# Performance work log

Measured on AMD Instinct MI355X. Metric: run time of the kernel, lower is better.

Reference implementation:

```python
import jax, jax.numpy as jnp
import numpy as np

B, S, H = 4, 2048, 1024
NH = 1                     # source code only type-checks with 1 head (see notes)
DH = H // NH               # head dim == hidden size
DT = 32                    # distance_type
LN_EPS = 1e-12


def setup_inputs() -> dict:
    key = jax.random.key(0)
    ks = jax.random.split(key, 12)
    sd = 0.02
    hidden_states = jax.random.normal(ks[0], (B, S, H), dtype=jnp.float32)
    attention_mask = jnp.zeros((B, 1, 1, S), dtype=jnp.float32)
    word_word_relation = jax.random.randint(ks[1], (B, S, S), 0, DT, dtype=jnp.int64)
    dist_emb = sd * jax.random.normal(ks[2], (DT, H), dtype=jnp.float32)
    dist_emb = dist_emb.at[0].set(0.0)  # padding_idx=0
    return {
        "hidden_states": hidden_states,
        "attention_mask": attention_mask,
        "word_word_relation": word_word_relation,
        "Wq": sd * jax.random.normal(ks[3], (H, H), dtype=jnp.float32),
        "bq": jnp.zeros((H,), dtype=jnp.float32),
        "Wk": sd * jax.random.normal(ks[4], (H, H), dtype=jnp.float32),
        "bk": jnp.zeros((H,), dtype=jnp.float32),
        "Wv": sd * jax.random.normal(ks[5], (H, H), dtype=jnp.float32),
        "bv": jnp.zeros((H,), dtype=jnp.float32),
        "dist_emb": dist_emb,
        "Wo": sd * jax.random.normal(ks[6], (H, H), dtype=jnp.float32),
        "bo": jnp.zeros((H,), dtype=jnp.float32),
        "ln_g": jnp.ones((H,), dtype=jnp.float32),
        "ln_b": jnp.zeros((H,), dtype=jnp.float32),
    }


def _split_heads(x):
    # [B,S,H] -> [B,NH,S,DH]
    return x.reshape(B, S, NH, DH).transpose(0, 2, 1, 3)


def reference(hidden_states, attention_mask, word_word_relation, Wq, bq, Wk, bk,
              Wv, bv, dist_emb, Wo, bo, ln_g, ln_b):
    q = _split_heads(hidden_states @ Wq.T + bq)   # [B,NH,S,DH]
    k = _split_heads(hidden_states @ Wk.T + bk)
    v = _split_heads(hidden_states @ Wv.T + bv)

    # raw QK^T scores [B,NH,S,S]
    scores = jnp.einsum('bhqd,bhkd->bhqk', q, k)

    # query . distance_embedding^T : [B,NH,S,DT]
    word_dot_distance = jnp.einsum('bhqd,td->bhqt', q, dist_emb)

    rel = word_word_relation[:, None, :, :]       # [B,1,S,S]
    # gather per-pair distance score along the distance-type axis
    dist_att = jnp.take_along_axis(word_dot_distance, rel, axis=3)  # [B,NH,S,S]
    mask_out = (rel == 1).astype(scores.dtype)    # keep only relation==1 pairs
    dist_att = dist_att * mask_out

    scores = (scores + dist_att) / jnp.sqrt(jnp.asarray(DH, scores.dtype))
    scores = scores + attention_mask              # additive BERT mask
    probs = jax.nn.softmax(scores, axis=-1)       # dropout p=0 -> identity

    ctx = jnp.einsum('bhqk,bhkd->bhqd', probs, v) # [B,NH,S,DH]
    ctx = ctx.transpose(0, 2, 1, 3).reshape(B, S, H)

    # BertSelfOutput: dense -> residual -> LayerNorm
    attn_out = ctx @ Wo.T + bo
    x = attn_out + hidden_states
    mu = jnp.mean(x, axis=-1, keepdims=True)
    var = jnp.mean(jnp.square(x - mu), axis=-1, keepdims=True)
    out = (x - mu) * jax.lax.rsqrt(var + LN_EPS) * ln_g + ln_b
    return out
```

## Files before the change

### kernel.cpp

```cpp
#include <hip/hip_runtime.h>

#define BM 128
#define BN 128
#define BKH 32

typedef __bf16 bf16x8 __attribute__((ext_vector_type(8)));
typedef __bf16 bf16x4 __attribute__((ext_vector_type(4)));
typedef float f32x4 __attribute__((ext_vector_type(4)));
typedef __bf16 bf16_t;

__device__ __forceinline__ void gl_lds16(const void* g, void* l) {
    __builtin_amdgcn_global_load_lds(
        (const __attribute__((address_space(1))) void*)g,
        (__attribute__((address_space(3))) void*)l, 16, 0, 0);
}

__global__ __launch_bounds__(256)
void cvt_all_kernel(const float* __restrict__ hid,
                    const float* __restrict__ w0, const float* __restrict__ w1,
                    const float* __restrict__ w2, const float* __restrict__ w3,
                    bf16_t* __restrict__ hidb, bf16_t* __restrict__ wb)
{
    const int bid = blockIdx.x;
    const float* src;
    bf16_t* dst;
    size_t off;
    if (bid < 8192) {
        src = hid; dst = hidb; off = (size_t)bid * 1024;
    } else {
        const int i = (bid - 8192) >> 10;
        src = (i == 0) ? w0 : (i == 1) ? w1 : (i == 2) ? w2 : w3;
        dst = wb + (size_t)i * 1024 * 1024;
        off = (size_t)((bid - 8192) & 1023) * 1024;
    }
    const size_t idx = off + threadIdx.x * 4;
    const float4 v = *(const float4*)(src + idx);
    bf16x4 o;
    o[0] = (__bf16)v.x; o[1] = (__bf16)v.y;
    o[2] = (__bf16)v.z; o[3] = (__bf16)v.w;
    *(bf16x4*)(dst + idx) = o;
}

template <int MODE, int SWIZ>
__global__ __launch_bounds__(256)
void gemm_bt(const bf16_t* __restrict__ A, const bf16_t* __restrict__ Bw,
             const float* __restrict__ bias, const float* __restrict__ bias2,
             const float* __restrict__ bias3,
             bf16_t* __restrict__ C, bf16_t* __restrict__ C2,
             int M, int N, int K,
             long long sAz, long long sBz, long long sCz,
             const float* __restrict__ resid,
             int Sdim, int DHdim)
{
    const int bz = blockIdx.z;
    const float* bi = bias;
    if (MODE == 0) {
        Bw += (long long)bz * N * K;
        bi = (bz == 0) ? bias : (bz == 1 ? bias2 : bias3);
        if (bz < 2) C += (long long)bz * sCz;
    } else {
        A += (long long)bz * sAz;
        Bw += (long long)bz * sBz;
        C += (long long)bz * sCz;
    }

    int m0, n0;
    if (SWIZ) {
        const int num_n = N / BN;
        const int pid = blockIdx.x;
        const int group = 8 * num_n;
        const int g = pid / group;
        m0 = (g * 8 + (pid % 8)) * BM;
        n0 = ((pid % group) / 8) * BN;
    } else {
        m0 = blockIdx.y * BM;
        n0 = blockIdx.x * BN;
    }
    const int tid = threadIdx.x;
    const int w = tid >> 6;
    const int lane = tid & 63;
    const int wr = w >> 1;
    const int wc = w & 1;
    const int srow = lane >> 2;
    const int scol = (lane & 3) * 8;
    const int frow = lane & 15;
    const int fk = (lane >> 4) * 8;

    __shared__ bf16_t smem[4 * BM * BKH];
    bf16_t* A0 = smem;
    bf16_t* A1 = smem + BM * BKH;
    bf16_t* B0 = smem + 2 * BM * BKH;
    bf16_t* B1 = smem + 3 * BM * BKH;

    f32x4 acc[4][4];
#pragma unroll
    for (int i = 0; i < 4; ++i)
#pragma unroll
        for (int j = 0; j < 4; ++j) acc[i][j] = (f32x4)0.0f;

    for (int k0 = 0; k0 < K; k0 += 2 * BKH) {
#pragma unroll
        for (int i = 0; i < 2; ++i) {
            const int r = i * 64 + w * 16;
            const bf16_t* ga = A + (size_t)(m0 + r + srow) * K + (k0 + scol);
            const bf16_t* gb = Bw + (size_t)(n0 + r + srow) * K + (k0 + scol);
            gl_lds16(ga,        &A0[r * BKH]);
            gl_lds16(ga + BKH,  &A1[r * BKH]);
            gl_lds16(gb,        &B0[r * BKH]);
            gl_lds16(gb + BKH,  &B1[r * BKH]);
        }
        __syncthreads();
#pragma unroll
        for (int h = 0; h < 2; ++h) {
            const bf16_t* Ah = h ? A1 : A0;
            const bf16_t* Bh = h ? B1 : B0;
            bf16x8 af[4], bfv[4];
#pragma unroll
            for (int t = 0; t < 4; ++t) {
                af[t]  = *(const bf16x8*)&Ah[(wr * 64 + t * 16 + frow) * BKH + fk];
                bfv[t] = *(const bf16x8*)&Bh[(wc * 64 + t * 16 + frow) * BKH + fk];
            }
#pragma unroll
            for (int mt = 0; mt < 4; ++mt)
#pragma unroll
                for (int nt = 0; nt < 4; ++nt)
                    acc[mt][nt] = __builtin_amdgcn_mfma_f32_16x16x32_bf16(
                        af[mt], bfv[nt], acc[mt][nt], 0, 0, 0);
        }
        __syncthreads();
    }

    const int crow = (lane >> 4) * 4;
    const int ccol = lane & 15;

    if (MODE == 0 && bz == 2) {
#pragma unroll
        for (int mt = 0; mt < 4; ++mt) {
            const int mb = m0 + wr * 64 + mt * 16 + crow;
#pragma unroll
            for (int nt = 0; nt < 4; ++nt) {
                const int n = n0 + wc * 64 + nt * 16 + ccol;
                const float bv = bi[n];
                const int b = mb >> 11;
                const int s = mb & 2047;
                union { ushort4 u; bf16_t h[4]; } pk;
#pragma unroll
                for (int r = 0; r < 4; ++r) pk.h[r] = (__bf16)(acc[mt][nt][r] + bv);
                *(ushort4*)&C2[(size_t)b * DHdim * Sdim + (size_t)n * Sdim + s] = pk.u;
            }
        }
        return;
    }

    bf16_t* tw = smem + w * (16 * 72);
    const int r0 = lane >> 3;
    const int cseg = (lane & 7) * 8;

    float bv[4];
    if (MODE == 0 || MODE == 4) {
#pragma unroll
        for (int nt = 0; nt < 4; ++nt)
            bv[nt] = bi[n0 + wc * 64 + nt * 16 + ccol];
    }

#pragma unroll
    for (int mt = 0; mt < 4; ++mt) {
#pragma unroll
        for (int nt = 0; nt < 4; ++nt) {
            const float badd = (MODE == 0 || MODE == 4) ? bv[nt] : 0.0f;
#pragma unroll
            for (int r = 0; r < 4; ++r)
                tw[(crow + r) * 72 + nt * 16 + ccol] = (__bf16)(acc[mt][nt][r] + badd);
        }
        bf16x8 va = *(const bf16x8*)&tw[r0 * 72 + cseg];
        bf16x8 vb = *(const bf16x8*)&tw[(r0 + 8) * 72 + cseg];

        const int gm_a = m0 + wr * 64 + mt * 16 + r0;
        const int gm_b = gm_a + 8;
        const int gn = n0 + wc * 64 + cseg;

        if (MODE == 0 || MODE == 3) {
            *(bf16x8*)&C[(size_t)gm_a * N + gn] = va;
            *(bf16x8*)&C[(size_t)gm_b * N + gn] = vb;
        } else {
            const float4 xa0 = *(const float4*)&resid[(size_t)gm_a * N + gn];
            const float4 xa1 = *(const float4*)&resid[(size_t)gm_a * N + gn + 4];
            const float4 xb0 = *(const float4*)&resid[(size_t)gm_b * N + gn];
            const float4 xb1 = *(const float4*)&resid[(size_t)gm_b * N + gn + 4];
            bf16x8 oa, ob;
            oa[0] = (__bf16)((float)va[0] + xa0.x);
            oa[1] = (__bf16)((float)va[1] + xa0.y);
            oa[2] = (__bf16)((float)va[2] + xa0.z);
            oa[3] = (__bf16)((float)va[3] + xa0.w);
            oa[4] = (__bf16)((float)va[4] + xa1.x);
            oa[5] = (__bf16)((float)va[5] + xa1.y);
            oa[6] = (__bf16)((float)va[6] + xa1.z);
            oa[7] = (__bf16)((float)va[7] + xa1.w);
            ob[0] = (__bf16)((float)vb[0] + xb0.x);
            ob[1] = (__bf16)((float)vb[1] + xb0.y);
            ob[2] = (__bf16)((float)vb[2] + xb0.z);
            ob[3] = (__bf16)((float)vb[3] + xb0.w);
            ob[4] = (__bf16)((float)vb[4] + xb1.x);
            ob[5] = (__bf16)((float)vb[5] + xb1.y);
            ob[6] = (__bf16)((float)vb[6] + xb1.z);
            ob[7] = (__bf16)((float)vb[7] + xb1.w);
            *(bf16x8*)&C[(size_t)gm_a * N + gn] = oa;
            *(bf16x8*)&C[(size_t)gm_b * N + gn] = ob;
        }
    }
}

__global__ __launch_bounds__(256)
void softmax_kernel(bf16_t* __restrict__ sc, const int* __restrict__ rel,
                    const bf16_t* __restrict__ q, const float* __restrict__ de,
                    const float* __restrict__ mask)
{
    constexpr int S = 2048, H = 1024;
    const int row = blockIdx.x;
    const int b = row >> 11;
    const int tid = threadIdx.x;
    const int w = tid >> 6, lane = tid & 63;
    __shared__ float rd1[4], rmax[4], rsum[4];

    const bf16x4 q4 = *(const bf16x4*)(q + (size_t)row * H + tid * 4);
    const float4 e4 = *(const float4*)(de + H + tid * 4);
    float pd = (float)q4[0] * e4.x + (float)q4[1] * e4.y
             + (float)q4[2] * e4.z + (float)q4[3] * e4.w;
#pragma unroll
    for (int off = 32; off; off >>= 1) pd += __shfl_xor(pd, off, 64);
    if (lane == 0) rd1[w] = pd;
    __syncthreads();
    const float d1s = (rd1[0] + rd1[1] + rd1[2] + rd1[3]) * 0.03125f;

    bf16_t* p = sc + (size_t)row * S;
    const bf16x8 x = *(const bf16x8*)(p + tid * 8);
    const int4 rl0 = *(const int4*)&rel[(size_t)row * S + tid * 8];
    const int4 rl1 = *(const int4*)&rel[(size_t)row * S + tid * 8 + 4];
    const float4 mk0 = *(const float4*)&mask[(size_t)b * S + tid * 8];
    const float4 mk1 = *(const float4*)&mask[(size_t)b * S + tid * 8 + 4];
    const int rls[8] = {rl0.x, rl0.y, rl0.z, rl0.w, rl1.x, rl1.y, rl1.z, rl1.w};
    const float mks[8] = {mk0.x, mk0.y, mk0.z, mk0.w, mk1.x, mk1.y, mk1.z, mk1.w};
    float v[8];
    float mx = -1e30f;
#pragma unroll
    for (int j = 0; j < 8; ++j) {
        v[j] = (float)x[j] * 0.03125f + mks[j] + (rls[j] == 1 ? d1s : 0.0f);
        mx = fmaxf(mx, v[j]);
    }
#pragma unroll
    for (int off = 32; off; off >>= 1) mx = fmaxf(mx, __shfl_xor(mx, off, 64));
    if (lane == 0) rmax[w] = mx;
    __syncthreads();
    mx = fmaxf(fmaxf(rmax[0], rmax[1]), fmaxf(rmax[2], rmax[3]));
    float sum = 0.0f;
#pragma unroll
    for (int j = 0; j < 8; ++j) { v[j] = __expf(v[j] - mx); sum += v[j]; }
#pragma unroll
    for (int off = 32; off; off >>= 1) sum += __shfl_xor(sum, off, 64);
    if (lane == 0) rsum[w] = sum;
    __syncthreads();
    sum = rsum[0] + rsum[1] + rsum[2] + rsum[3];
    const float inv = 1.0f / sum;
    bf16x8 o;
#pragma unroll
    for (int j = 0; j < 8; ++j) o[j] = (__bf16)(v[j] * inv);
    *(bf16x8*)(p + tid * 8) = o;
}

__global__ __launch_bounds__(256)
void ln_kernel(const bf16_t* __restrict__ x, const float* __restrict__ gamma,
               const float* __restrict__ beta, float* __restrict__ out)
{
    const int H = 1024;
    const size_t row = blockIdx.x;
    const int tid = threadIdx.x;
    const int w = tid >> 6, lane = tid & 63;
    bf16x4 xv = *(const bf16x4*)(x + row * H + tid * 4);
    float v[4] = {(float)xv[0], (float)xv[1], (float)xv[2], (float)xv[3]};
    float s = 0.0f, s2 = 0.0f;
#pragma unroll
    for (int j = 0; j < 4; ++j) { s += v[j]; s2 += v[j] * v[j]; }
#pragma unroll
    for (int off = 32; off; off >>= 1) {
        s += __shfl_xor(s, off, 64);
        s2 += __shfl_xor(s2, off, 64);
    }
    __shared__ float rs[4], rs2[4];
    if (lane == 0) { rs[w] = s; rs2[w] = s2; }
    __syncthreads();
    s  = rs[0] + rs[1] + rs[2] + rs[3];
    s2 = rs2[0] + rs2[1] + rs2[2] + rs2[3];
    const float mu  = s * (1.0f / H);
    const float var = s2 * (1.0f / H) - mu * mu;
    const float inv = rsqrtf(var + 1e-12f);
    float4 o;
    const int c = tid * 4;
    o.x = (v[0] - mu) * inv * gamma[c + 0] + beta[c + 0];
    o.y = (v[1] - mu) * inv * gamma[c + 1] + beta[c + 1];
    o.z = (v[2] - mu) * inv * gamma[c + 2] + beta[c + 2];
    o.w = (v[3] - mu) * inv * gamma[c + 3] + beta[c + 3];
    *(float4*)(out + row * H + tid * 4) = o;
}

extern "C" void kernel_launch(void* const* d_in, const int* in_sizes, int n_in,
                              void* d_out, int out_size, void* d_ws, size_t ws_size,
                              hipStream_t stream)
{
    constexpr int B = 4, S = 2048, H = 1024;
    const float* hid = (const float*)d_in[0];
    const float* am  = (const float*)d_in[1];
    const int*   rel = (const int*)d_in[2];
    const float* Wq  = (const float*)d_in[3];
    const float* bq  = (const float*)d_in[4];
    const float* Wk  = (const float*)d_in[5];
    const float* bk  = (const float*)d_in[6];
    const float* Wv  = (const float*)d_in[7];
    const float* bv  = (const float*)d_in[8];
    const float* de  = (const float*)d_in[9];
    const float* Wo  = (const float*)d_in[10];
    const float* bo  = (const float*)d_in[11];
    const float* lng = (const float*)d_in[12];
    const float* lnb = (const float*)d_in[13];
    float* out = (float*)d_out;

    char* ws = (char*)d_ws;
    const int n_tok = B * S;
    const size_t MB = 1024 * 1024;
    bf16_t* hidb = (bf16_t*)(ws);
    bf16_t* Wqb  = (bf16_t*)(ws + 16 * MB);
    bf16_t* Wob  = (bf16_t*)(ws + 22 * MB);
    bf16_t* qb   = (bf16_t*)(ws + 24 * MB);
    bf16_t* kb   = (bf16_t*)(ws + 40 * MB);
    bf16_t* vT   = (bf16_t*)(ws + 56 * MB);
    bf16_t* ctx  = (bf16_t*)(ws + 72 * MB);
    bf16_t* sc   = (bf16_t*)(ws + 88 * MB);
    bf16_t* xb   = (bf16_t*)(ws + 88 * MB);

    const dim3 blk(256);
    cvt_all_kernel<<<dim3(8192 + 4 * 1024), blk, 0, stream>>>(
        hid, Wq, Wk, Wv, Wo, hidb, Wqb);

    gemm_bt<0, 1><<<dim3(64 * 8, 1, 3), blk, 0, stream>>>(
        hidb, Wqb, bq, bk, bv, qb, vT, n_tok, H, H,
        0, 0, (long long)n_tok * H,
        nullptr, S, H);
    gemm_bt<3, 0><<<dim3(S / BN, S / BM, B), blk, 0, stream>>>(
        qb, kb, nullptr, nullptr, nullptr, sc, nullptr, S, S, H,
        (long long)S * H, (long long)S * H, (long long)S * S,
        nullptr, S, H);
    softmax_kernel<<<dim3(B * S), blk, 0, stream>>>(sc, rel, qb, de, am);
    gemm_bt<3, 0><<<dim3(H / BN, S / BM, B), blk, 0, stream>>>(
        sc, vT, nullptr, nullptr, nullptr, ctx, nullptr, S, H, S,
        (long long)S * S, (long long)H * S, (long long)S * H,
        nullptr, S, H);
    gemm_bt<4, 0><<<dim3(H / BN, n_tok / BM, 1), blk, 0, stream>>>(
        ctx, Wob, bo, nullptr, nullptr, xb, nullptr, n_tok, H, H, 0, 0, 0,
        hid, S, H);
    ln_kernel<<<dim3(n_tok), blk, 0, stream>>>(xb, lng, lnb, out);
}
```

Measured before the change: 379.3 us.

## Rework GEMM into 256x128 tiles with triple-buffered swizzled LDS pipeline

```diff
diff --git a/kernel.cpp b/kernel.cpp
--- a/kernel.cpp
+++ b/kernel.cpp
@@ -1,18 +1,25 @@
 #include <hip/hip_runtime.h>
 
-#define BM 128
+#define BM 256
 #define BN 128
-#define BKH 32
+#define BK 64
+#define NBUF 3
+#define BUFELEMS ((BM + BN) * BK)
 
 typedef __bf16 bf16x8 __attribute__((ext_vector_type(8)));
 typedef __bf16 bf16x4 __attribute__((ext_vector_type(4)));
 typedef float f32x4 __attribute__((ext_vector_type(4)));
 typedef __bf16 bf16_t;
 
+#define MFMA16(a, b, c) __builtin_amdgcn_mfma_f32_16x16x32_bf16((a), (b), (c), 0, 0, 0)
+
 __device__ __forceinline__ void gl_lds16(const void* g, void* l) {
     __builtin_amdgcn_global_load_lds(
         (const __attribute__((address_space(1))) void*)g,
         (__attribute__((address_space(3))) void*)l, 16, 0, 0);
+}
+__device__ __forceinline__ void barrier_mem() {
+    asm volatile("s_barrier" ::: "memory");
 }
 
 __global__ __launch_bounds__(256)
@@ -41,8 +48,8 @@
     *(bf16x4*)(dst + idx) = o;
 }
 
-template <int MODE, int SWIZ>
-__global__ __launch_bounds__(256)
+template <int MODE>
+__global__ __launch_bounds__(512, 2)
 void gemm_bt(const bf16_t* __restrict__ A, const bf16_t* __restrict__ Bw,
              const float* __restrict__ bias, const float* __restrict__ bias2,
              const float* __restrict__ bias3,
@@ -63,34 +70,33 @@
         Bw += (long long)bz * sBz;
         C += (long long)bz * sCz;
     }
-
-    int m0, n0;
-    if (SWIZ) {
-        const int num_n = N / BN;
-        const int pid = blockIdx.x;
-        const int group = 8 * num_n;
-        const int g = pid / group;
-        m0 = (g * 8 + (pid % 8)) * BM;
-        n0 = ((pid % group) / 8) * BN;
-    } else {
-        m0 = blockIdx.y * BM;
-        n0 = blockIdx.x * BN;
-    }
+    const int m0 = blockIdx.y * BM;
+    const int n0 = blockIdx.x * BN;
+
     const int tid = threadIdx.x;
     const int w = tid >> 6;
     const int lane = tid & 63;
     const int wr = w >> 1;
     const int wc = w & 1;
-    const int srow = lane >> 2;
-    const int scol = (lane & 3) * 8;
     const int frow = lane & 15;
-    const int fk = (lane >> 4) * 8;
-
-    __shared__ bf16_t smem[4 * BM * BKH];
-    bf16_t* A0 = smem;
-    bf16_t* A1 = smem + BM * BKH;
-    bf16_t* B0 = smem + 2 * BM * BKH;
-    bf16_t* B1 = smem + 3 * BM * BKH;
+    const int fchunk = lane >> 4;
+
+    __shared__ bf16_t smem[NBUF * BUFELEMS];
+
+    const int srow8 = lane >> 3;
+    const int sch = (lane & 7) ^ srow8;
+    const size_t soff = (size_t)(w * 8 + srow8) * K + ((size_t)sch << 3);
+    const bf16_t* gA = A + (size_t)m0 * K;
+    const bf16_t* gB = Bw + (size_t)n0 * K;
+
+    auto stA = [&](int kt, int b, int i) {
+        gl_lds16(gA + (size_t)(i * 64) * K + (size_t)kt * BK + soff,
+                 smem + (size_t)b * BUFELEMS + (i * 64 + w * 8) * BK);
+    };
+    auto stB = [&](int kt, int b, int i) {
+        gl_lds16(gB + (size_t)(i * 64) * K + (size_t)kt * BK + soff,
+                 smem + (size_t)b * BUFELEMS + BM * BK + (i * 64 + w * 8) * BK);
+    };
 
     f32x4 acc[4][4];
 #pragma unroll
@@ -98,36 +104,78 @@
 #pragma unroll
         for (int j = 0; j < 4; ++j) acc[i][j] = (f32x4)0.0f;
 
-    for (int k0 = 0; k0 < K; k0 += 2 * BKH) {
-#pragma unroll
-        for (int i = 0; i < 2; ++i) {
-            const int r = i * 64 + w * 16;
-            const bf16_t* ga = A + (size_t)(m0 + r + srow) * K + (k0 + scol);
-            const bf16_t* gb = Bw + (size_t)(n0 + r + srow) * K + (k0 + scol);
-            gl_lds16(ga,        &A0[r * BKH]);
-            gl_lds16(ga + BKH,  &A1[r * BKH]);
-            gl_lds16(gb,        &B0[r * BKH]);
-            gl_lds16(gb + BKH,  &B1[r * BKH]);
-        }
-        __syncthreads();
-#pragma unroll
-        for (int h = 0; h < 2; ++h) {
-            const bf16_t* Ah = h ? A1 : A0;
-            const bf16_t* Bh = h ? B1 : B0;
-            bf16x8 af[4], bfv[4];
-#pragma unroll
-            for (int t = 0; t < 4; ++t) {
-                af[t]  = *(const bf16x8*)&Ah[(wr * 64 + t * 16 + frow) * BKH + fk];
-                bfv[t] = *(const bf16x8*)&Bh[(wc * 64 + t * 16 + frow) * BKH + fk];
+    const int NT = K / BK;
+
+#pragma unroll
+    for (int i = 0; i < 4; ++i) stA(0, 0, i);
+#pragma unroll
+    for (int i = 0; i < 2; ++i) stB(0, 0, i);
+#pragma unroll
+    for (int i = 0; i < 4; ++i) stA(1, 1, i);
+#pragma unroll
+    for (int i = 0; i < 2; ++i) stB(1, 1, i);
+
+    for (int kt = 0; kt < NT; ++kt) {
+        const int cur = kt % NBUF;
+        const int nxt = (kt + 2) % NBUF;
+        const bool pf = (kt + 2 < NT);
+        if (pf) { stA(kt + 2, nxt, 0); stA(kt + 2, nxt, 1); stA(kt + 2, nxt, 2); }
+        if (pf)               asm volatile("s_waitcnt vmcnt(9)" ::: "memory");
+        else if (kt + 1 < NT) asm volatile("s_waitcnt vmcnt(6)" ::: "memory");
+        else                  asm volatile("s_waitcnt vmcnt(0)" ::: "memory");
+        barrier_mem();
+
+        const bf16_t* Ab = smem + (size_t)cur * BUFELEMS;
+        const bf16_t* Bb = Ab + BM * BK;
+        const int sw = frow & 7;
+
+        bf16x8 af[4][2], b0v[2][2];
+#pragma unroll
+        for (int t = 0; t < 4; ++t) {
+            const int row = wr * 64 + t * 16 + frow;
+#pragma unroll
+            for (int kh = 0; kh < 2; ++kh)
+                af[t][kh] = *(const bf16x8*)&Ab[row * BK + (((kh * 4 + fchunk) ^ sw) << 3)];
+        }
+#pragma unroll
+        for (int u = 0; u < 2; ++u) {
+            const int row = wc * 64 + u * 16 + frow;
+#pragma unroll
+            for (int kh = 0; kh < 2; ++kh)
+                b0v[u][kh] = *(const bf16x8*)&Bb[row * BK + (((kh * 4 + fchunk) ^ sw) << 3)];
+        }
+        if (pf) { stA(kt + 2, nxt, 3); stB(kt + 2, nxt, 0); stB(kt + 2, nxt, 1); }
+
+        __builtin_amdgcn_s_setprio(1);
+#pragma unroll
+        for (int t = 0; t < 4; ++t)
+#pragma unroll
+            for (int u = 0; u < 2; ++u) {
+                acc[t][u] = MFMA16(af[t][0], b0v[u][0], acc[t][u]);
+                acc[t][u] = MFMA16(af[t][1], b0v[u][1], acc[t][u]);
             }
-#pragma unroll
-            for (int mt = 0; mt < 4; ++mt)
-#pragma unroll
-                for (int nt = 0; nt < 4; ++nt)
-                    acc[mt][nt] = __builtin_amdgcn_mfma_f32_16x16x32_bf16(
-                        af[mt], bfv[nt], acc[mt][nt], 0, 0, 0);
-        }
-        __syncthreads();
+        __builtin_amdgcn_s_setprio(0);
+
+        bf16x8 b1v[2][2];
+#pragma unroll
+        for (int u = 0; u < 2; ++u) {
+            const int row = wc * 64 + (u + 2) * 16 + frow;
+#pragma unroll
+            for (int kh = 0; kh < 2; ++kh)
+                b1v[u][kh] = *(const bf16x8*)&Bb[row * BK + (((kh * 4 + fchunk) ^ sw) << 3)];
+        }
+        barrier_mem();
+
+        __builtin_amdgcn_s_setprio(1);
+#pragma unroll
+        for (int t = 0; t < 4; ++t)
+#pragma unroll
+            for (int u = 0; u < 2; ++u) {
+                acc[t][u + 2] = MFMA16(af[t][0], b1v[u][0], acc[t][u + 2]);
+                acc[t][u + 2] = MFMA16(af[t][1], b1v[u][1], acc[t][u + 2]);
+            }
+        __builtin_amdgcn_s_setprio(0);
+        barrier_mem();
     }
 
     const int crow = (lane >> 4) * 4;
@@ -140,12 +188,12 @@
 #pragma unroll
             for (int nt = 0; nt < 4; ++nt) {
                 const int n = n0 + wc * 64 + nt * 16 + ccol;
-                const float bv = bi[n];
+                const float bvv = bi[n];
                 const int b = mb >> 11;
                 const int s = mb & 2047;
                 union { ushort4 u; bf16_t h[4]; } pk;
 #pragma unroll
-                for (int r = 0; r < 4; ++r) pk.h[r] = (__bf16)(acc[mt][nt][r] + bv);
+                for (int r = 0; r < 4; ++r) pk.h[r] = (__bf16)(acc[mt][nt][r] + bvv);
                 *(ushort4*)&C2[(size_t)b * DHdim * Sdim + (size_t)n * Sdim + s] = pk.u;
             }
         }
@@ -337,23 +385,24 @@
     bf16_t* xb   = (bf16_t*)(ws + 88 * MB);
 
     const dim3 blk(256);
+    const dim3 blkg(512);
     cvt_all_kernel<<<dim3(8192 + 4 * 1024), blk, 0, stream>>>(
         hid, Wq, Wk, Wv, Wo, hidb, Wqb);
 
-    gemm_bt<0, 1><<<dim3(64 * 8, 1, 3), blk, 0, stream>>>(
+    gemm_bt<0><<<dim3(H / BN, n_tok / BM, 3), blkg, 0, stream>>>(
         hidb, Wqb, bq, bk, bv, qb, vT, n_tok, H, H,
         0, 0, (long long)n_tok * H,
         nullptr, S, H);
-    gemm_bt<3, 0><<<dim3(S / BN, S / BM, B), blk, 0, stream>>>(
+    gemm_bt<3><<<dim3(S / BN, S / BM, B), blkg, 0, stream>>>(
         qb, kb, nullptr, nullptr, nullptr, sc, nullptr, S, S, H,
         (long long)S * H, (long long)S * H, (long long)S * S,
         nullptr, S, H);
     softmax_kernel<<<dim3(B * S), blk, 0, stream>>>(sc, rel, qb, de, am);
-    gemm_bt<3, 0><<<dim3(H / BN, S / BM, B), blk, 0, stream>>>(
+    gemm_bt<3><<<dim3(H / BN, S / BM, B), blkg, 0, stream>>>(
         sc, vT, nullptr, nullptr, nullptr, ctx, nullptr, S, H, S,
         (long long)S * S, (long long)H * S, (long long)S * H,
         nullptr, S, H);
-    gemm_bt<4, 0><<<dim3(H / BN, n_tok / BM, 1), blk, 0, stream>>>(
+    gemm_bt<4><<<dim3(H / BN, n_tok / BM, 1), blkg, 0, stream>>>(
         ctx, Wob, bo, nullptr, nullptr, xb, nullptr, n_tok, H, H, 0, 0, 0,
         hid, S, H);
     ln_kernel<<<dim3(n_tok), blk, 0, stream>>>(xb, lng, lnb, out);
```

Result: faster. 366.3 us (-3.4%).
